# Performance work log

Hardware: AMD Instinct MI355X
Metric: run time of the kernel (lower is better)

Reference implementation:

```python
import jax, jax.numpy as jnp
import numpy as np

UNITS = 1024
INPUT_DIM = 2048
OUTPUT_DIM = 1000
EPS = 0.01
DT = 0.1
BATCH = 8192


def _kaiming_like(key, shape, fan_in):
    # matches torch kaiming_uniform_(a=sqrt(5)) bound = sqrt(6/((1+5)*fan_in)) = 1/sqrt(fan_in)
    bound = 1.0 / np.sqrt(fan_in)
    return jax.random.uniform(key, shape, jnp.float32, -bound, bound)


def setup_inputs() -> dict:
    key = jax.random.key(0)
    ks = jax.random.split(key, 12)
    x = jax.random.normal(ks[0], (BATCH, INPUT_DIM), jnp.float32)
    W_in = _kaiming_like(ks[1], (UNITS, INPUT_DIM), INPUT_DIM)
    b_in = _kaiming_like(ks[2], (UNITS,), INPUT_DIM)
    W1 = _kaiming_like(ks[3], (UNITS, UNITS), UNITS)
    b1 = _kaiming_like(ks[4], (UNITS,), UNITS)
    W2 = _kaiming_like(ks[5], (UNITS, UNITS), UNITS)
    b2 = _kaiming_like(ks[6], (UNITS,), UNITS)
    W3 = _kaiming_like(ks[7], (UNITS, UNITS), UNITS)
    b3 = _kaiming_like(ks[8], (UNITS,), UNITS)
    W_out = _kaiming_like(ks[9], (OUTPUT_DIM, UNITS), UNITS)
    b_out = _kaiming_like(ks[10], (OUTPUT_DIM,), UNITS)
    return {"x": x, "W_in": W_in, "b_in": b_in, "W1": W1, "b1": b1,
            "W2": W2, "b2": b2, "W3": W3, "b3": b3,
            "W_out": W_out, "b_out": b_out}


def transnet_layer(z, W, b):
    # z: (B, 2U). Implicit layer: A y = rhs, output = C y - rhs (== -y mathematically)
    U = W.shape[0]
    u_in, v_in = z[:, :U], z[:, U:]
    relu_u = jax.nn.relu(u_in)
    rhs_u = u_in + DT * b                      # (B, U)
    rhs_v = v_in + (DT / EPS) * relu_u         # (B, U)
    rhs = jnp.concatenate([rhs_u, rhs_v], axis=1)  # (B, 2U)
    eye = jnp.eye(U, dtype=z.dtype)
    A = jnp.block([[eye, DT * W],
                   [-DT * W.T, (1.0 + DT / EPS) * eye]])  # (2U, 2U), batch-independent
    # factor once, solve against all batch rhs columns at once
    y = jnp.linalg.solve(A, rhs.T).T           # (B, 2U)
    u, v = y[:, :U], y[:, U:]
    u_out = DT * (v @ W.T) - u_in - DT * b
    v_out = -DT * (u @ W) + (DT / EPS) * v - v_in - (DT / EPS) * relu_u
    return jnp.concatenate([u_out, v_out], axis=1)


def reference(x, W_in, b_in, W1, b1, W2, b2, W3, b3, W_out, b_out):
    z = x @ W_in.T + b_in                      # (B, U)
    z = jnp.concatenate([z, jax.nn.relu(z)], axis=1)  # (B, 2U)
    z = transnet_layer(z, W1, b1)
    z = transnet_layer(z, W2, b2)
    z = transnet_layer(z, W3, b3)
    z = z[:, :UNITS]
    logits = jax.nn.softmax(z @ W_out.T + b_out, axis=1)
    return logits
```

## Files before the change

kernel.cpp:

```cpp
#include <hip/hip_runtime.h>
#include <hip/hip_bf16.h>
#include <cstdint>


typedef __bf16 bf16;
typedef __bf16 bf16x4 __attribute__((ext_vector_type(4)));
typedef __bf16 bf16x8 __attribute__((ext_vector_type(8)));
typedef float  f32x4  __attribute__((ext_vector_type(4)));

#define C_DT    0.1f
#define C_DTEPS 10.0f
#define C_DINV  (1.0f/11.0f)
#define C_MSC   (0.01f/121.0f)

__device__ __forceinline__ void async_load16(const bf16* g, bf16* l) {
    __builtin_amdgcn_global_load_lds(
        (__attribute__((address_space(1))) void*)(g),
        (__attribute__((address_space(3))) void*)(l),
        16, 0, 0);
}

__device__ __forceinline__ void remap_block(int& bx, int& by) {
    if (gridDim.y == 64) {
        const int lin  = by * 8 + bx;
        const int xcd  = lin & 7;
        const int slot = lin >> 3;
        by = xcd * 8 + (slot & 7);
        bx = slot >> 3;
    }
}

template<int EPI>
__global__ __launch_bounds__(256, 3)
void gemm_bt(const bf16* __restrict__ A, const bf16* __restrict__ B,
             float* __restrict__ out_f,
             bf16* __restrict__ out_b1, bf16* __restrict__ out_b2,
             const float* __restrict__ e0, const float* __restrict__ e1,
             const float* __restrict__ e2,
             int M, int N, int K, int lda, int ldb,
             int ldf, int ld1, int ld2, float sgn,
             long zsA, long zsB, long zs1, long zs2)
{
    __shared__ __attribute__((aligned(16))) char smem[32768];
    bf16* sAe = (bf16*)smem;
    bf16* sBe = (bf16*)(smem + 16384);

    const int t    = threadIdx.x;
    const int wave = t >> 6;
    const int lane = t & 63;
    int bx = blockIdx.x, by = blockIdx.y;
    remap_block(bx, by);
    const long zb = blockIdx.z;
    A += zb * zsA;
    B += zb * zsB;
    if (out_b1) out_b1 += zb * zs1;
    if (out_b2) out_b2 += zb * zs2;

    const long row0 = (long)by * 128;
    const long col0 = (long)bx * 128;
    const int wr = wave >> 1, wc = wave & 1;

    f32x4 acc[4][4];
#pragma unroll
    for (int i = 0; i < 4; i++)
#pragma unroll
        for (int j = 0; j < 4; j++)
            acc[i][j] = f32x4{0.f, 0.f, 0.f, 0.f};

    const int  q  = t >> 2;
    const int  gp = ((t & 3) + 4 - ((q + (q >> 2)) & 3)) & 3;
    const bf16* gA = A + (row0 + q) * (long)lda + gp * 8;
    const bf16* gB = B + (col0 + q) * (long)ldb + gp * 8;

    const int l15  = lane & 15;
    const int fch  = ((lane >> 4) + l15 + (l15 >> 2)) & 3;
    const int aoff = (wr * 64 + l15) * 32 + fch * 8;
    const int boff = (wc * 64 + l15) * 32 + fch * 8;

    auto stage = [&](int buf, int k0) {
        bf16* dA = sAe + buf * 4096 + wave * 512;
        bf16* dB = sBe + buf * 4096 + wave * 512;
        async_load16(gA + k0,                     dA);
        async_load16(gA + 64 * (long)lda + k0,    dA + 2048);
        async_load16(gB + k0,                     dB);
        async_load16(gB + 64 * (long)ldb + k0,    dB + 2048);
    };

    const int nIter = K >> 5;
    stage(0, 0);
    __syncthreads();
    for (int k = 0; k < nIter; k++) {
        const int cur = k & 1;
        if (k + 1 < nIter) stage(cur ^ 1, (k + 1) << 5);

        bf16x8 af[4], bfv[4];
#pragma unroll
        for (int i = 0; i < 4; i++)
            af[i] = *(const bf16x8*)(sAe + cur * 4096 + aoff + i * 16 * 32);
#pragma unroll
        for (int j = 0; j < 4; j++)
            bfv[j] = *(const bf16x8*)(sBe + cur * 4096 + boff + j * 16 * 32);
#pragma unroll
        for (int i = 0; i < 4; i++)
#pragma unroll
            for (int j = 0; j < 4; j++)
                acc[i][j] = __builtin_amdgcn_mfma_f32_16x16x32_bf16(
                    af[i], bfv[j], acc[i][j], 0, 0, 0);

        __syncthreads();
    }

    float* epi = (float*)smem + wave * 1024;
    const int wbase = (lane >> 4) * 256 + (l15 >> 2) * 4 + (l15 & 3);

#pragma unroll
    for (int i = 0; i < 4; i++) {
#pragma unroll
        for (int j = 0; j < 4; j++)
#pragma unroll
            for (int r = 0; r < 4; r++)
                epi[wbase + r * 64 + 16 * j] = acc[i][j][r];

#pragma unroll
        for (int qq = 0; qq < 4; qq++) {
            const f32x4 a4 = ((const f32x4*)epi)[qq * 64 + lane];
            const long m = row0 + wr * 64 + i * 16 + qq * 4 + (lane >> 4);
            const long n = col0 + wc * 64 + 4 * l15;

            if (EPI == 0) {
                const f32x4 b1 = *(const f32x4*)(e1 + n);
                const f32x4 b2 = *(const f32x4*)(e2 + n);
                f32x4 tv; bf16x4 rv, hv;
#pragma unroll
                for (int e = 0; e < 4; e++) {
                    tv[e] = a4[e] + b1[e];
                    rv[e] = (bf16)(11.f * fmaxf(tv[e], 0.f));
                    hv[e] = (bf16)(tv[e] + C_DT * b2[e]);
                }
                *(f32x4*)(out_f + m * (long)ldf + n)    = tv;
                *(bf16x4*)(out_b1 + m * (long)ld1 + n)  = rv;
                *(bf16x4*)(out_b2 + m * (long)ld2 + n)  = hv;
            } else if (EPI == 1) {
                bf16x4 ov;
#pragma unroll
                for (int e = 0; e < 4; e++)
                    ov[e] = (bf16)(((m == n + e) ? C_DINV : 0.f) - C_MSC * a4[e]);
                *(bf16x4*)(out_b1 + m * (long)ld1 + n) = ov;
                *(bf16x4*)(out_b2 + m * (long)ld2 + n) = ov;
            } else if (EPI == 2) {
                bf16x4 ov, o2;
#pragma unroll
                for (int e = 0; e < 4; e++) {
                    ov[e] = (bf16)(sgn * a4[e]);
                    o2[e] = (bf16)(C_DT * sgn * a4[e]);
                }
                *(bf16x4*)(out_b1 + m * (long)ld1 + n) = ov;
                if (out_b2) *(bf16x4*)(out_b2 + m * (long)ld2 + n) = o2;
            } else {
                const f32x4 u0 = *(const f32x4*)(e0 + m * (long)ldf + n);
                const f32x4 b1 = *(const f32x4*)(e1 + n);
                bf16x4 hv, lv;
#pragma unroll
                for (int e = 0; e < 4; e++) {
                    float un = sgn * a4[e] - u0[e] - C_DT * b1[e];
                    bf16 h = (bf16)un;
                    hv[e] = h;
                    lv[e] = (bf16)(un - (float)h);
                }
                *(bf16x4*)(out_b1 + m * (long)ld1 + n) = hv;
                *(bf16x4*)(out_b2 + m * (long)ld2 + n) = lv;
            }
        }
    }
}

__global__ __launch_bounds__(256, 2)
void gemm_layer(const bf16* __restrict__ A, const bf16* __restrict__ B1,
                const bf16* __restrict__ B2, float* __restrict__ u,
                bf16* __restrict__ ACo,
                const float* __restrict__ bl, const float* __restrict__ bn)
{
    __shared__ __attribute__((aligned(16))) char smem[49152];
    bf16* sA  = (bf16*)smem;
    bf16* sB1 = (bf16*)(smem + 16384);
    bf16* sB2 = (bf16*)(smem + 32768);

    const int t    = threadIdx.x;
    const int wave = t >> 6;
    const int lane = t & 63;
    int bx = blockIdx.x, by = blockIdx.y;
    remap_block(bx, by);
    const long row0 = (long)by * 128;
    const long col0 = (long)bx * 128;
    const int wr = wave >> 1, wc = wave & 1;

    f32x4 accU[4][4], accV[4][4];
#pragma unroll
    for (int i = 0; i < 4; i++)
#pragma unroll
        for (int j = 0; j < 4; j++) {
            accU[i][j] = f32x4{0.f, 0.f, 0.f, 0.f};
            accV[i][j] = f32x4{0.f, 0.f, 0.f, 0.f};
        }

    const int  q  = t >> 2;
    const int  gp = ((t & 3) + 4 - ((q + (q >> 2)) & 3)) & 3;
    const bf16* gA  = A  + (row0 + q) * 2048 + gp * 8;
    const bf16* gB1 = B1 + (col0 + q) * 2048 + gp * 8;
    const bf16* gB2 = B2 + (col0 + q) * 2048 + gp * 8;

    const int l15  = lane & 15;
    const int fch  = ((lane >> 4) + l15 + (l15 >> 2)) & 3;
    const int aoff = (wr * 64 + l15) * 32 + fch * 8;
    const int boff = (wc * 64 + l15) * 32 + fch * 8;

    auto stage = [&](int buf, int k0) {
        bf16* dA  = sA  + buf * 4096 + wave * 512;
        bf16* dB1 = sB1 + buf * 4096 + wave * 512;
        bf16* dB2 = sB2 + buf * 4096 + wave * 512;
        async_load16(gA  + k0,             dA);
        async_load16(gA  + 64 * 2048 + k0, dA + 2048);
        async_load16(gB1 + k0,             dB1);
        async_load16(gB1 + 64 * 2048 + k0, dB1 + 2048);
        async_load16(gB2 + k0,             dB2);
        async_load16(gB2 + 64 * 2048 + k0, dB2 + 2048);
    };

    stage(0, 0);
    __syncthreads();
    for (int k = 0; k < 64; k++) {
        const int cur = k & 1;
        if (k + 1 < 64) stage(cur ^ 1, (k + 1) << 5);

        bf16x8 af[4], b1v[4], b2v[4];
#pragma unroll
        for (int i = 0; i < 4; i++)
            af[i] = *(const bf16x8*)(sA + cur * 4096 + aoff + i * 16 * 32);
#pragma unroll
        for (int j = 0; j < 4; j++) {
            b1v[j] = *(const bf16x8*)(sB1 + cur * 4096 + boff + j * 16 * 32);
            b2v[j] = *(const bf16x8*)(sB2 + cur * 4096 + boff + j * 16 * 32);
        }
#pragma unroll
        for (int i = 0; i < 4; i++)
#pragma unroll
            for (int j = 0; j < 4; j++) {
                accV[i][j] = __builtin_amdgcn_mfma_f32_16x16x32_bf16(
                    af[i], b1v[j], accV[i][j], 0, 0, 0);
                accU[i][j] = __builtin_amdgcn_mfma_f32_16x16x32_bf16(
                    af[i], b2v[j], accU[i][j], 0, 0, 0);
            }
        __syncthreads();
    }

    float* epi = (float*)smem + wave * 1024;
    const int wbase = (lane >> 4) * 256 + (l15 >> 2) * 4 + (l15 & 3);

#pragma unroll
    for (int i = 0; i < 4; i++) {
#pragma unroll
        for (int j = 0; j < 4; j++)
#pragma unroll
            for (int r = 0; r < 4; r++)
                epi[wbase + r * 64 + 16 * j] = accV[i][j][r];
        f32x4 v4[4];
#pragma unroll
        for (int qq = 0; qq < 4; qq++)
            v4[qq] = ((const f32x4*)epi)[qq * 64 + lane];
#pragma unroll
        for (int j = 0; j < 4; j++)
#pragma unroll
            for (int r = 0; r < 4; r++)
                epi[wbase + r * 64 + 16 * j] = accU[i][j][r];

#pragma unroll
        for (int qq = 0; qq < 4; qq++) {
            const f32x4 a4 = ((const f32x4*)epi)[qq * 64 + lane];
            const long m  = row0 + wr * 64 + i * 16 + qq * 4 + (lane >> 4);
            const long n  = col0 + wc * 64 + 4 * l15;
            const long iu = m * 1024 + n;
            const f32x4 u0 = *(const f32x4*)(u + iu);
            const f32x4 c1 = *(const f32x4*)(bl + n);
            const f32x4 c2 = *(const f32x4*)(bn + n);
            f32x4 un; bf16x4 rv, hv;
#pragma unroll
            for (int e = 0; e < 4; e++) {
                un[e] = a4[e] - u0[e] - C_DT * c1[e];
                rv[e] = (bf16)(C_DTEPS * fmaxf(un[e], 0.f) - v4[qq][e]);
                hv[e] = (bf16)(un[e] + C_DT * c2[e]);
            }
            *(f32x4*)(u + iu) = un;
            *(bf16x4*)(ACo + m * 2048 + n)        = rv;
            *(bf16x4*)(ACo + m * 2048 + 1024 + n) = hv;
        }
    }
}

__global__ __launch_bounds__(256, 3)
void gemm_step67(const bf16* __restrict__ Minv, const bf16* __restrict__ Wbf,
                 bf16* __restrict__ Bc1, bf16* __restrict__ Pm,
                 bf16* __restrict__ Cc)
{
    __shared__ __attribute__((aligned(16))) char smem[32768];
    bf16* sAe = (bf16*)smem;
    bf16* sBe = (bf16*)(smem + 16384);

    const int t    = threadIdx.x;
    const int wave = t >> 6;
    const int lane = t & 63;
    const int bx = blockIdx.x, by = blockIdx.y;
    const long zb = blockIdx.z;
    const long M1v = 1024L * 1024;

    const bf16 *A, *B;
    bf16 *o1, *o2;
    int ld1;
    const bool alt = (zb >= 3);
    if (!alt) {
        A = Minv + zb * M1v; B = Wbf + zb * M1v;
        o1 = Bc1 + zb * 2 * M1v; o2 = nullptr; ld1 = 2048;
    } else {
        const long zr = zb - 3;
        A = Wbf + zr * M1v; B = Minv + zr * M1v;
        o1 = Pm + zr * M1v; o2 = Cc + zr * 2 * M1v; ld1 = 1024;
    }

    const long row0 = (long)by * 128;
    const long col0 = (long)bx * 128;
    const int wr = wave >> 1, wc = wave & 1;

    f32x4 acc[4][4];
#pragma unroll
    for (int i = 0; i < 4; i++)
#pragma unroll
        for (int j = 0; j < 4; j++)
            acc[i][j] = f32x4{0.f, 0.f, 0.f, 0.f};

    const int  q  = t >> 2;
    const int  gp = ((t & 3) + 4 - ((q + (q >> 2)) & 3)) & 3;
    const bf16* gA = A + (row0 + q) * 1024 + gp * 8;
    const bf16* gB = B + (col0 + q) * 1024 + gp * 8;

    const int l15  = lane & 15;
    const int fch  = ((lane >> 4) + l15 + (l15 >> 2)) & 3;
    const int aoff = (wr * 64 + l15) * 32 + fch * 8;
    const int boff = (wc * 64 + l15) * 32 + fch * 8;

    auto stage = [&](int buf, int k0) {
        bf16* dA = sAe + buf * 4096 + wave * 512;
        bf16* dB = sBe + buf * 4096 + wave * 512;
        async_load16(gA + k0,              dA);
        async_load16(gA + 64 * 1024 + k0,  dA + 2048);
        async_load16(gB + k0,              dB);
        async_load16(gB + 64 * 1024 + k0,  dB + 2048);
    };

    stage(0, 0);
    __syncthreads();
    for (int k = 0; k < 32; k++) {
        const int cur = k & 1;
        if (k + 1 < 32) stage(cur ^ 1, (k + 1) << 5);

        bf16x8 af[4], bfv[4];
#pragma unroll
        for (int i = 0; i < 4; i++)
            af[i] = *(const bf16x8*)(sAe + cur * 4096 + aoff + i * 16 * 32);
#pragma unroll
        for (int j = 0; j < 4; j++)
            bfv[j] = *(const bf16x8*)(sBe + cur * 4096 + boff + j * 16 * 32);
#pragma unroll
        for (int i = 0; i < 4; i++)
#pragma unroll
            for (int j = 0; j < 4; j++)
                acc[i][j] = __builtin_amdgcn_mfma_f32_16x16x32_bf16(
                    af[i], bfv[j], acc[i][j], 0, 0, 0);
        __syncthreads();
    }

    float* epi = (float*)smem + wave * 1024;
    const int wbase = (lane >> 4) * 256 + (l15 >> 2) * 4 + (l15 & 3);

#pragma unroll
    for (int i = 0; i < 4; i++) {
#pragma unroll
        for (int j = 0; j < 4; j++)
#pragma unroll
            for (int r = 0; r < 4; r++)
                epi[wbase + r * 64 + 16 * j] = acc[i][j][r];

#pragma unroll
        for (int qq = 0; qq < 4; qq++) {
            const f32x4 a4 = ((const f32x4*)epi)[qq * 64 + lane];
            const long m = row0 + wr * 64 + i * 16 + qq * 4 + (lane >> 4);
            const long n = col0 + wc * 64 + 4 * l15;
            if (!alt) {
                bf16x4 ov;
#pragma unroll
                for (int e = 0; e < 4; e++) ov[e] = (bf16)(C_DT * a4[e]);
                *(bf16x4*)(o1 + m * (long)ld1 + n) = ov;
            } else {
                bf16x4 ov, o2v;
#pragma unroll
                for (int e = 0; e < 4; e++) {
                    ov[e]  = (bf16)a4[e];
                    o2v[e] = (bf16)(C_DT * a4[e]);
                }
                *(bf16x4*)(o1 + m * (long)ld1 + n) = ov;
                *(bf16x4*)(o2 + m * 2048 + n)      = o2v;
            }
        }
    }
}

__global__ __launch_bounds__(256, 2)
void gemm_split(const bf16* __restrict__ Ah, const bf16* __restrict__ Al,
                const bf16* __restrict__ Bh, const bf16* __restrict__ Bl,
                float* __restrict__ out, const float* __restrict__ bias,
                int M, int N, int K, int blim)
{
    __shared__ __attribute__((aligned(16))) char smem[65536];
    bf16* sAh = (bf16*)smem;
    bf16* sAl = (bf16*)(smem + 16384);
    bf16* sBh = (bf16*)(smem + 32768);
    bf16* sBl = (bf16*)(smem + 49152);

    const int t    = threadIdx.x;
    const int wave = t >> 6;
    const int lane = t & 63;
    int bx = blockIdx.x, by = blockIdx.y;
    remap_block(bx, by);
    const long row0 = (long)by * 128;
    const long col0 = (long)bx * 128;
    const int wr = wave >> 1, wc = wave & 1;

    f32x4 acc[4][4];
#pragma unroll
    for (int i = 0; i < 4; i++)
#pragma unroll
        for (int j = 0; j < 4; j++)
            acc[i][j] = f32x4{0.f, 0.f, 0.f, 0.f};

    const int  q  = t >> 2;
    const int  gp = ((t & 3) + 4 - ((q + (q >> 2)) & 3)) & 3;
    const long gao = (row0 + q) * (long)K + gp * 8;
    const long gbo = (col0 + q) * (long)K + gp * 8;

    const int l15  = lane & 15;
    const int fch  = ((lane >> 4) + l15 + (l15 >> 2)) & 3;
    const int aoff = (wr * 64 + l15) * 32 + fch * 8;
    const int boff = (wc * 64 + l15) * 32 + fch * 8;

    auto stage = [&](int buf, int k0) {
        const int d = buf * 4096 + wave * 512;
        async_load16(Ah + gao + k0,                 sAh + d);
        async_load16(Ah + gao + 64 * (long)K + k0,  sAh + d + 2048);
        async_load16(Al + gao + k0,                 sAl + d);
        async_load16(Al + gao + 64 * (long)K + k0,  sAl + d + 2048);
        async_load16(Bh + gbo + k0,                 sBh + d);
        async_load16(Bh + gbo + 64 * (long)K + k0,  sBh + d + 2048);
        async_load16(Bl + gbo + k0,                 sBl + d);
        async_load16(Bl + gbo + 64 * (long)K + k0,  sBl + d + 2048);
    };

    const int nIter = K >> 5;
    stage(0, 0);
    __syncthreads();
    for (int k = 0; k < nIter; k++) {
        const int cur = k & 1;
        if (k + 1 < nIter) stage(cur ^ 1, (k + 1) << 5);

        bf16x8 ah[4], al[4], bh[4], bl[4];
#pragma unroll
        for (int i = 0; i < 4; i++) {
            ah[i] = *(const bf16x8*)(sAh + cur * 4096 + aoff + i * 16 * 32);
            al[i] = *(const bf16x8*)(sAl + cur * 4096 + aoff + i * 16 * 32);
        }
#pragma unroll
        for (int j = 0; j < 4; j++) {
            bh[j] = *(const bf16x8*)(sBh + cur * 4096 + boff + j * 16 * 32);
            bl[j] = *(const bf16x8*)(sBl + cur * 4096 + boff + j * 16 * 32);
        }
#pragma unroll
        for (int i = 0; i < 4; i++)
#pragma unroll
            for (int j = 0; j < 4; j++) {
                acc[i][j] = __builtin_amdgcn_mfma_f32_16x16x32_bf16(
                    ah[i], bh[j], acc[i][j], 0, 0, 0);
                acc[i][j] = __builtin_amdgcn_mfma_f32_16x16x32_bf16(
                    ah[i], bl[j], acc[i][j], 0, 0, 0);
                acc[i][j] = __builtin_amdgcn_mfma_f32_16x16x32_bf16(
                    al[i], bh[j], acc[i][j], 0, 0, 0);
            }
        __syncthreads();
    }

    float* epi = (float*)smem + wave * 1024;
    const int wbase = (lane >> 4) * 256 + (l15 >> 2) * 4 + (l15 & 3);

#pragma unroll
    for (int i = 0; i < 4; i++) {
#pragma unroll
        for (int j = 0; j < 4; j++)
#pragma unroll
            for (int r = 0; r < 4; r++)
                epi[wbase + r * 64 + 16 * j] = acc[i][j][r];

#pragma unroll
        for (int qq = 0; qq < 4; qq++) {
            f32x4 a4 = ((const f32x4*)epi)[qq * 64 + lane];
            const long m = row0 + wr * 64 + i * 16 + qq * 4 + (lane >> 4);
            const long n = col0 + wc * 64 + 4 * l15;
            f32x4 bv = f32x4{0.f, 0.f, 0.f, 0.f};
            if (n < blim) bv = *(const f32x4*)(bias + n);
#pragma unroll
            for (int e = 0; e < 4; e++) a4[e] += bv[e];
            *(f32x4*)(out + m * (long)N + n) = a4;
        }
    }
}

__global__ __launch_bounds__(256)
void prep_all(const float* __restrict__ x, bf16* __restrict__ xb,
              const float* __restrict__ win, bf16* __restrict__ winb,
              const float* __restrict__ wout, bf16* __restrict__ wouth,
              bf16* __restrict__ woutl,
              const float* __restrict__ w0, const float* __restrict__ w1,
              const float* __restrict__ w2,
              bf16* __restrict__ Wb, bf16* __restrict__ Wtb)
{
    __shared__ float tile[32][33];
    const long bid = blockIdx.x;
    const int  t   = threadIdx.x;

    if (bid < 16384) {
        const long i4 = bid * 256 + t;
        const f32x4 v = ((const f32x4*)x)[i4];
        bf16x4 o;
#pragma unroll
        for (int e = 0; e < 4; e++) o[e] = (bf16)v[e];
        ((bf16x4*)xb)[i4] = o;
    } else if (bid < 18432) {
        const long i4 = (bid - 16384) * 256 + t;
        const f32x4 v = ((const f32x4*)win)[i4];
        bf16x4 o;
#pragma unroll
        for (int e = 0; e < 4; e++) o[e] = (bf16)v[e];
        ((bf16x4*)winb)[i4] = o;
    } else if (bid < 19456) {
        const long i4   = (bid - 18432) * 256 + t;
        const long base = i4 * 4;
        const int  nrow = (int)(base >> 10);
        bf16x4 h, l;
        if (nrow < 1000) {
            const f32x4 v = ((const f32x4*)wout)[i4];
#pragma unroll
            for (int e = 0; e < 4; e++) {
                bf16 hh = (bf16)v[e];
                h[e] = hh;
                l[e] = (bf16)(v[e] - (float)hh);
            }
        } else {
#pragma unroll
            for (int e = 0; e < 4; e++) { h[e] = (bf16)0.f; l[e] = (bf16)0.f; }
        }
        ((bf16x4*)wouth)[i4] = h;
        ((bf16x4*)woutl)[i4] = l;
    } else {
        const long b2 = bid - 19456;
        const int  z  = (int)(b2 >> 10);
        const int  idx = (int)(b2 & 1023);
        const float* W = (z == 0) ? w0 : (z == 1) ? w1 : w2;
        const long zo = (long)z << 20;
        const int bxt = (idx & 31) * 32, byt = (idx >> 5) * 32;
        const int tx = t & 31, ty = t >> 5;
#pragma unroll
        for (int i = 0; i < 32; i += 8) {
            float v = W[(long)(byt + ty + i) * 1024 + bxt + tx];
            tile[ty + i][tx] = v;
            Wb[zo + (long)(byt + ty + i) * 1024 + bxt + tx] = (bf16)v;
        }
        __syncthreads();
#pragma unroll
        for (int i = 0; i < 32; i += 8)
            Wtb[zo + (long)(bxt + ty + i) * 1024 + byt + tx] = (bf16)tile[tx][ty + i];
    }
}

__global__ __launch_bounds__(256)
void softmax_rows(const float* __restrict__ logits, float* __restrict__ out)
{
    const int row = blockIdx.x;
    const float* lp = logits + (long)row * 1024;
    const int t = threadIdx.x;
    float v[4];
    float mx = -1e30f;
#pragma unroll
    for (int i = 0; i < 4; i++) {
        const int c = t + i * 256;
        v[i] = (c < 1000) ? lp[c] : -1e30f;
        mx = fmaxf(mx, v[i]);
    }
#pragma unroll
    for (int off = 32; off; off >>= 1)
        mx = fmaxf(mx, __shfl_xor(mx, off));
    __shared__ float sm[4], ss[4];
    const int wave = t >> 6;
    if ((t & 63) == 0) sm[wave] = mx;
    __syncthreads();
    mx = fmaxf(fmaxf(sm[0], sm[1]), fmaxf(sm[2], sm[3]));
    float sum = 0.f;
#pragma unroll
    for (int i = 0; i < 4; i++) {
        v[i] = __expf(v[i] - mx);
        sum += v[i];
    }
#pragma unroll
    for (int off = 32; off; off >>= 1)
        sum += __shfl_xor(sum, off);
    if ((t & 63) == 0) ss[wave] = sum;
    __syncthreads();
    const float inv = 1.f / (ss[0] + ss[1] + ss[2] + ss[3]);
#pragma unroll
    for (int i = 0; i < 4; i++) {
        const int c = t + i * 256;
        if (c < 1000) out[(long)row * 1000 + c] = v[i] * inv;
    }
}

extern "C" void kernel_launch(void* const* d_in, const int* in_sizes, int n_in,
                              void* d_out, int out_size, void* d_ws, size_t ws_size,
                              hipStream_t stream)
{
    const float* x     = (const float*)d_in[0];
    const float* W_in  = (const float*)d_in[1];
    const float* b_in  = (const float*)d_in[2];
    const float* Ws[3] = {(const float*)d_in[3], (const float*)d_in[5], (const float*)d_in[7]};
    const float* bs[3] = {(const float*)d_in[4], (const float*)d_in[6], (const float*)d_in[8]};
    const float* W_out = (const float*)d_in[9];
    const float* b_out = (const float*)d_in[10];
    float* out = (float*)d_out;

    char* ws = (char*)d_ws;
    const size_t MB = 1u << 20;
    const long M1 = 1024L * 1024;
    bf16*  xb    = (bf16*)(ws);
    bf16*  Minv  = (bf16*)(ws +  6 * MB);
    bf16*  Pmat  = (bf16*)(ws + 12 * MB);
    bf16*  Bcat  = (bf16*)(ws + 18 * MB);
    bf16*  zh    = (bf16*)(ws);
    bf16*  zl    = (bf16*)(ws + 16 * MB);
    bf16*  Winb  = (bf16*)(ws + 32 * MB);
    bf16*  Wouth = (bf16*)(ws + 36 * MB);
    bf16*  Woutl = (bf16*)(ws + 38 * MB);
    bf16*  Wbf   = (bf16*)(ws + 40 * MB);
    bf16*  Ccat  = (bf16*)(ws + 46 * MB);
    float* u     = (float*)(ws + 58 * MB);
    float* logits= (float*)(ws + 58 * MB);
    bf16*  AC_a  = (bf16*)(ws + 90 * MB);
    bf16*  AC_b  = (bf16*)(ws + 122 * MB);
    bf16*  Wtbf  = (bf16*)(ws + 122 * MB);

    const dim3 blk(256);
    const dim3 gBig(8, 64);
    const dim3 gSm3(8, 8, 3);
    const dim3 gSm6(8, 8, 6);

    prep_all<<<22528, blk, 0, stream>>>(x, xb, W_in, Winb, W_out, Wouth, Woutl,
                                        Ws[0], Ws[1], Ws[2], Wbf, Wtbf);

    gemm_bt<0><<<gBig, blk, 0, stream>>>(xb, Winb, u, AC_a, AC_a + 1024,
                                         nullptr, b_in, bs[0],
                                         8192, 1024, 2048, 2048, 2048,
                                         1024, 2048, 2048, 1.f, 0, 0, 0, 0);

    gemm_bt<1><<<gSm3, blk, 0, stream>>>(Wtbf, Wtbf, nullptr, Minv, Bcat,
                                         nullptr, nullptr, nullptr,
                                         1024, 1024, 1024, 1024, 1024,
                                         0, 1024, 2048, 1.f, M1, M1, M1, 2 * M1);
    gemm_step67<<<gSm6, blk, 0, stream>>>(Minv, Wbf, Bcat + 1024, Pmat, Ccat);
    gemm_bt<2><<<gSm3, blk, 0, stream>>>(Pmat, Wbf, nullptr, Ccat + 1024, nullptr,
                                         nullptr, nullptr, nullptr,
                                         1024, 1024, 1024, 1024, 1024,
                                         0, 2048, 0, 0.01f, M1, M1, 2 * M1, 0);

    gemm_layer<<<gBig, blk, 0, stream>>>(AC_a, Bcat, Ccat, u, AC_b, bs[0], bs[1]);
    gemm_layer<<<gBig, blk, 0, stream>>>(AC_b, Bcat + 2 * M1, Ccat + 2 * M1,
                                         u, AC_a, bs[1], bs[2]);
    gemm_bt<5><<<gBig, blk, 0, stream>>>(AC_a, Ccat + 4 * M1, nullptr, zh, zl,
                                         u, bs[2], nullptr,
                                         8192, 1024, 2048, 2048, 2048,
                                         1024, 1024, 1024, 1.f, 0, 0, 0, 0);

    gemm_split<<<gBig, blk, 0, stream>>>(zh, zl, Wouth, Woutl, logits, b_out,
                                         8192, 1024, 1024, 1000);
    softmax_rows<<<8192, blk, 0, stream>>>(logits, out);
}
```

Baseline: 515.3 us.

## Compute layer U from materialized V via W instead of separate wide GEMM

Each implicit layer is split into two GEMMs. The first computes V with K=2048 and writes it to a bf16 buffer. The second GEMM has K=1024 and multiplies V by W to get the U term, scaled by DT in the epilogue. This replaces the fused dual-accumulator GEMM, which computed both halves over K=2048 each, and it cuts precomputation of the Pmat/Ccat matrices to only the final layer's slice. The cost is an extra bf16 round trip of V through global memory, one more kernel launch per layer, and V being rounded to bf16 before it feeds U, which can reduce accuracy.

```diff
diff --git a/kernel.cpp b/kernel.cpp
--- a/kernel.cpp
+++ b/kernel.cpp
@@ -174,16 +174,14 @@
     }
 }
 
-__global__ __launch_bounds__(256, 2)
-void gemm_layer(const bf16* __restrict__ A, const bf16* __restrict__ B1,
-                const bf16* __restrict__ B2, float* __restrict__ u,
-                bf16* __restrict__ ACo,
-                const float* __restrict__ bl, const float* __restrict__ bn)
+__global__ __launch_bounds__(256, 3)
+void gemm_ulayer(const bf16* __restrict__ V, const bf16* __restrict__ W,
+                 float* __restrict__ u, bf16* __restrict__ ACo,
+                 const float* __restrict__ bl, const float* __restrict__ bn)
 {
-    __shared__ __attribute__((aligned(16))) char smem[49152];
-    bf16* sA  = (bf16*)smem;
-    bf16* sB1 = (bf16*)(smem + 16384);
-    bf16* sB2 = (bf16*)(smem + 32768);
+    __shared__ __attribute__((aligned(16))) char smem[32768];
+    bf16* sAe = (bf16*)smem;
+    bf16* sBe = (bf16*)(smem + 16384);
 
     const int t    = threadIdx.x;
     const int wave = t >> 6;
@@ -194,20 +192,17 @@
     const long col0 = (long)bx * 128;
     const int wr = wave >> 1, wc = wave & 1;
 
-    f32x4 accU[4][4], accV[4][4];
+    f32x4 acc[4][4];
 #pragma unroll
     for (int i = 0; i < 4; i++)
 #pragma unroll
-        for (int j = 0; j < 4; j++) {
-            accU[i][j] = f32x4{0.f, 0.f, 0.f, 0.f};
-            accV[i][j] = f32x4{0.f, 0.f, 0.f, 0.f};
-        }
+        for (int j = 0; j < 4; j++)
+            acc[i][j] = f32x4{0.f, 0.f, 0.f, 0.f};
 
     const int  q  = t >> 2;
     const int  gp = ((t & 3) + 4 - ((q + (q >> 2)) & 3)) & 3;
-    const bf16* gA  = A  + (row0 + q) * 2048 + gp * 8;
-    const bf16* gB1 = B1 + (col0 + q) * 2048 + gp * 8;
-    const bf16* gB2 = B2 + (col0 + q) * 2048 + gp * 8;
+    const bf16* gA = V + (row0 + q) * 1024 + gp * 8;
+    const bf16* gB = W + (col0 + q) * 1024 + gp * 8;
 
     const int l15  = lane & 15;
     const int fch  = ((lane >> 4) + l15 + (l15 >> 2)) & 3;
@@ -215,41 +210,33 @@
     const int boff = (wc * 64 + l15) * 32 + fch * 8;
 
     auto stage = [&](int buf, int k0) {
-        bf16* dA  = sA  + buf * 4096 + wave * 512;
-        bf16* dB1 = sB1 + buf * 4096 + wave * 512;
-        bf16* dB2 = sB2 + buf * 4096 + wave * 512;
-        async_load16(gA  + k0,             dA);
-        async_load16(gA  + 64 * 2048 + k0, dA + 2048);
-        async_load16(gB1 + k0,             dB1);
-        async_load16(gB1 + 64 * 2048 + k0, dB1 + 2048);
-        async_load16(gB2 + k0,             dB2);
-        async_load16(gB2 + 64 * 2048 + k0, dB2 + 2048);
+        bf16* dA = sAe + buf * 4096 + wave * 512;
+        bf16* dB = sBe + buf * 4096 + wave * 512;
+        async_load16(gA + k0,              dA);
+        async_load16(gA + 64 * 1024 + k0,  dA + 2048);
+        async_load16(gB + k0,              dB);
+        async_load16(gB + 64 * 1024 + k0,  dB + 2048);
     };
 
     stage(0, 0);
     __syncthreads();
-    for (int k = 0; k < 64; k++) {
+    for (int k = 0; k < 32; k++) {
         const int cur = k & 1;
-        if (k + 1 < 64) stage(cur ^ 1, (k + 1) << 5);
-
-        bf16x8 af[4], b1v[4], b2v[4];
+        if (k + 1 < 32) stage(cur ^ 1, (k + 1) << 5);
+
+        bf16x8 af[4], bfv[4];
 #pragma unroll
         for (int i = 0; i < 4; i++)
-            af[i] = *(const bf16x8*)(sA + cur * 4096 + aoff + i * 16 * 32);
-#pragma unroll
-        for (int j = 0; j < 4; j++) {
-            b1v[j] = *(const bf16x8*)(sB1 + cur * 4096 + boff + j * 16 * 32);
-            b2v[j] = *(const bf16x8*)(sB2 + cur * 4096 + boff + j * 16 * 32);
-        }
+            af[i] = *(const bf16x8*)(sAe + cur * 4096 + aoff + i * 16 * 32);
+#pragma unroll
+        for (int j = 0; j < 4; j++)
+            bfv[j] = *(const bf16x8*)(sBe + cur * 4096 + boff + j * 16 * 32);
 #pragma unroll
         for (int i = 0; i < 4; i++)
 #pragma unroll
-            for (int j = 0; j < 4; j++) {
-                accV[i][j] = __builtin_amdgcn_mfma_f32_16x16x32_bf16(
-                    af[i], b1v[j], accV[i][j], 0, 0, 0);
-                accU[i][j] = __builtin_amdgcn_mfma_f32_16x16x32_bf16(
-                    af[i], b2v[j], accU[i][j], 0, 0, 0);
-            }
+            for (int j = 0; j < 4; j++)
+                acc[i][j] = __builtin_amdgcn_mfma_f32_16x16x32_bf16(
+                    af[i], bfv[j], acc[i][j], 0, 0, 0);
         __syncthreads();
     }
 
@@ -262,16 +249,7 @@
         for (int j = 0; j < 4; j++)
 #pragma unroll
             for (int r = 0; r < 4; r++)
-                epi[wbase + r * 64 + 16 * j] = accV[i][j][r];
-        f32x4 v4[4];
-#pragma unroll
-        for (int qq = 0; qq < 4; qq++)
-            v4[qq] = ((const f32x4*)epi)[qq * 64 + lane];
-#pragma unroll
-        for (int j = 0; j < 4; j++)
-#pragma unroll
-            for (int r = 0; r < 4; r++)
-                epi[wbase + r * 64 + 16 * j] = accU[i][j][r];
+                epi[wbase + r * 64 + 16 * j] = acc[i][j][r];
 
 #pragma unroll
         for (int qq = 0; qq < 4; qq++) {
@@ -279,14 +257,15 @@
             const long m  = row0 + wr * 64 + i * 16 + qq * 4 + (lane >> 4);
             const long n  = col0 + wc * 64 + 4 * l15;
             const long iu = m * 1024 + n;
-            const f32x4 u0 = *(const f32x4*)(u + iu);
-            const f32x4 c1 = *(const f32x4*)(bl + n);
-            const f32x4 c2 = *(const f32x4*)(bn + n);
+            const f32x4  u0 = *(const f32x4*)(u + iu);
+            const f32x4  c1 = *(const f32x4*)(bl + n);
+            const f32x4  c2 = *(const f32x4*)(bn + n);
+            const bf16x4 vv = *(const bf16x4*)(V + iu);
             f32x4 un; bf16x4 rv, hv;
 #pragma unroll
             for (int e = 0; e < 4; e++) {
-                un[e] = a4[e] - u0[e] - C_DT * c1[e];
-                rv[e] = (bf16)(C_DTEPS * fmaxf(un[e], 0.f) - v4[qq][e]);
+                un[e] = C_DT * a4[e] - u0[e] - C_DT * c1[e];
+                rv[e] = (bf16)(C_DTEPS * fmaxf(un[e], 0.f) - (float)vv[e]);
                 hv[e] = (bf16)(un[e] + C_DT * c2[e]);
             }
             *(f32x4*)(u + iu) = un;
@@ -315,14 +294,13 @@
     const bf16 *A, *B;
     bf16 *o1, *o2;
     int ld1;
-    const bool alt = (zb >= 3);
+    const bool alt = (zb >= 2);
     if (!alt) {
         A = Minv + zb * M1v; B = Wbf + zb * M1v;
         o1 = Bc1 + zb * 2 * M1v; o2 = nullptr; ld1 = 2048;
     } else {
-        const long zr = zb - 3;
-        A = Wbf + zr * M1v; B = Minv + zr * M1v;
-        o1 = Pm + zr * M1v; o2 = Cc + zr * 2 * M1v; ld1 = 1024;
+        A = Wbf + 2 * M1v; B = Minv + 2 * M1v;
+        o1 = Pm; o2 = Cc; ld1 = 1024;
     }
 
     const long row0 = (long)by * 128;
@@ -644,6 +622,7 @@
     const size_t MB = 1u << 20;
     const long M1 = 1024L * 1024;
     bf16*  xb    = (bf16*)(ws);
+    bf16*  Vbuf  = (bf16*)(ws);
     bf16*  Minv  = (bf16*)(ws +  6 * MB);
     bf16*  Pmat  = (bf16*)(ws + 12 * MB);
     bf16*  Bcat  = (bf16*)(ws + 18 * MB);
@@ -663,7 +642,7 @@
     const dim3 blk(256);
     const dim3 gBig(8, 64);
     const dim3 gSm3(8, 8, 3);
-    const dim3 gSm6(8, 8, 6);
+    const dim3 gSm1(8, 8, 1);
 
     prep_all<<<22528, blk, 0, stream>>>(x, xb, W_in, Winb, W_out, Wouth, Woutl,
                                         Ws[0], Ws[1], Ws[2], Wbf, Wtbf);
@@ -677,16 +656,25 @@
                                          nullptr, nullptr, nullptr,
                                          1024, 1024, 1024, 1024, 1024,
                                          0, 1024, 2048, 1.f, M1, M1, M1, 2 * M1);
-    gemm_step67<<<gSm6, blk, 0, stream>>>(Minv, Wbf, Bcat + 1024, Pmat, Ccat);
-    gemm_bt<2><<<gSm3, blk, 0, stream>>>(Pmat, Wbf, nullptr, Ccat + 1024, nullptr,
+    gemm_step67<<<gSm3, blk, 0, stream>>>(Minv, Wbf, Bcat + 1024, Pmat, Ccat);
+    gemm_bt<2><<<gSm1, blk, 0, stream>>>(Pmat, Wbf + 2 * M1, nullptr,
+                                         Ccat + 1024, nullptr,
                                          nullptr, nullptr, nullptr,
                                          1024, 1024, 1024, 1024, 1024,
-                                         0, 2048, 0, 0.01f, M1, M1, 2 * M1, 0);
-
-    gemm_layer<<<gBig, blk, 0, stream>>>(AC_a, Bcat, Ccat, u, AC_b, bs[0], bs[1]);
-    gemm_layer<<<gBig, blk, 0, stream>>>(AC_b, Bcat + 2 * M1, Ccat + 2 * M1,
-                                         u, AC_a, bs[1], bs[2]);
-    gemm_bt<5><<<gBig, blk, 0, stream>>>(AC_a, Ccat + 4 * M1, nullptr, zh, zl,
+                                         0, 2048, 0, 0.01f, 0, 0, 0, 0);
+
+    gemm_bt<2><<<gBig, blk, 0, stream>>>(AC_a, Bcat, nullptr, Vbuf, nullptr,
+                                         nullptr, nullptr, nullptr,
+                                         8192, 1024, 2048, 2048, 2048,
+                                         0, 1024, 0, 1.f, 0, 0, 0, 0);
+    gemm_ulayer<<<gBig, blk, 0, stream>>>(Vbuf, Wbf, u, AC_b, bs[0], bs[1]);
+    gemm_bt<2><<<gBig, blk, 0, stream>>>(AC_b, Bcat + 2 * M1, nullptr, Vbuf, nullptr,
+                                         nullptr, nullptr, nullptr,
+                                         8192, 1024, 2048, 2048, 2048,
+                                         0, 1024, 0, 1.f, 0, 0, 0, 0);
+    gemm_ulayer<<<gBig, blk, 0, stream>>>(Vbuf, Wbf + M1, u, AC_a, bs[1], bs[2]);
+
+    gemm_bt<5><<<gBig, blk, 0, stream>>>(AC_a, Ccat, nullptr, zh, zl,
                                          u, bs[2], nullptr,
                                          8192, 1024, 2048, 2048, 2048,
                                          1024, 1024, 1024, 1.f, 0, 0, 0, 0);
```

New measurement: 531.0 us. +3.1%, slower.

## Merge first-layer and matrix-inverse GEMMs; fuse prep GEMMs via atomic dependency counter

Applied to the files above, without the earlier changes.

Runs the input projection GEMM and the three per-layer Minv Gram GEMMs in one launch, with block roles chosen by blockIdx.y, so the small 1024x1024 GEMMs fill idle CUs alongside the big one. It also collapses the step67 and EPI2 GEMMs into a single persistent-style launch. Consumer blocks spin on a global atomic counter until all 384 producer blocks have finished. Producer blocks also copy Minv into the Bcat high half, replacing the duplicate write in the old epilogue. This removes several launches and tail effects, but the spin-wait assumes producer blocks are scheduled before consumers and can deadlock if they are not; it also adds a memset.

```diff
diff --git a/kernel.cpp b/kernel.cpp
--- a/kernel.cpp
+++ b/kernel.cpp
@@ -127,36 +127,7 @@
             const long m = row0 + wr * 64 + i * 16 + qq * 4 + (lane >> 4);
             const long n = col0 + wc * 64 + 4 * l15;
 
-            if (EPI == 0) {
-                const f32x4 b1 = *(const f32x4*)(e1 + n);
-                const f32x4 b2 = *(const f32x4*)(e2 + n);
-                f32x4 tv; bf16x4 rv, hv;
-#pragma unroll
-                for (int e = 0; e < 4; e++) {
-                    tv[e] = a4[e] + b1[e];
-                    rv[e] = (bf16)(11.f * fmaxf(tv[e], 0.f));
-                    hv[e] = (bf16)(tv[e] + C_DT * b2[e]);
-                }
-                *(f32x4*)(out_f + m * (long)ldf + n)    = tv;
-                *(bf16x4*)(out_b1 + m * (long)ld1 + n)  = rv;
-                *(bf16x4*)(out_b2 + m * (long)ld2 + n)  = hv;
-            } else if (EPI == 1) {
-                bf16x4 ov;
-#pragma unroll
-                for (int e = 0; e < 4; e++)
-                    ov[e] = (bf16)(((m == n + e) ? C_DINV : 0.f) - C_MSC * a4[e]);
-                *(bf16x4*)(out_b1 + m * (long)ld1 + n) = ov;
-                *(bf16x4*)(out_b2 + m * (long)ld2 + n) = ov;
-            } else if (EPI == 2) {
-                bf16x4 ov, o2;
-#pragma unroll
-                for (int e = 0; e < 4; e++) {
-                    ov[e] = (bf16)(sgn * a4[e]);
-                    o2[e] = (bf16)(C_DT * sgn * a4[e]);
-                }
-                *(bf16x4*)(out_b1 + m * (long)ld1 + n) = ov;
-                if (out_b2) *(bf16x4*)(out_b2 + m * (long)ld2 + n) = o2;
-            } else {
+            if (EPI == 5) {
                 const f32x4 u0 = *(const f32x4*)(e0 + m * (long)ldf + n);
                 const f32x4 b1 = *(const f32x4*)(e1 + n);
                 bf16x4 hv, lv;
@@ -171,6 +142,284 @@
                 *(bf16x4*)(out_b2 + m * (long)ld2 + n) = lv;
             }
         }
+    }
+}
+
+__global__ __launch_bounds__(256, 3)
+void gemm_z0m(const bf16* __restrict__ xb, const bf16* __restrict__ winb,
+              const bf16* __restrict__ wtbf,
+              float* __restrict__ u, bf16* __restrict__ ACa,
+              bf16* __restrict__ Minv,
+              const float* __restrict__ e1, const float* __restrict__ e2)
+{
+    __shared__ __attribute__((aligned(16))) char smem[32768];
+    bf16* sAe = (bf16*)smem;
+    bf16* sBe = (bf16*)(smem + 16384);
+
+    const int t    = threadIdx.x;
+    const int wave = t >> 6;
+    const int lane = t & 63;
+    const long M1v = 1024L * 1024;
+
+    const bool mainp = (blockIdx.y < 64);
+    int bx, by, nIter, zm = 0;
+    long lda;
+    const bf16 *Abase, *Bbase;
+    if (mainp) {
+        const int lin  = blockIdx.y * 8 + blockIdx.x;
+        const int xcd  = lin & 7;
+        const int slot = lin >> 3;
+        by = xcd * 8 + (slot & 7);
+        bx = slot >> 3;
+        lda = 2048; nIter = 64;
+        Abase = xb; Bbase = winb;
+    } else {
+        zm = (blockIdx.y - 64) >> 3;
+        by = (blockIdx.y - 64) & 7;
+        bx = blockIdx.x;
+        lda = 1024; nIter = 32;
+        Abase = wtbf + zm * M1v; Bbase = Abase;
+    }
+    const long row0 = (long)by * 128;
+    const long col0 = (long)bx * 128;
+    const int wr = wave >> 1, wc = wave & 1;
+
+    f32x4 acc[4][4];
+#pragma unroll
+    for (int i = 0; i < 4; i++)
+#pragma unroll
+        for (int j = 0; j < 4; j++)
+            acc[i][j] = f32x4{0.f, 0.f, 0.f, 0.f};
+
+    const int  q  = t >> 2;
+    const int  gp = ((t & 3) + 4 - ((q + (q >> 2)) & 3)) & 3;
+    const bf16* gA = Abase + (row0 + q) * lda + gp * 8;
+    const bf16* gB = Bbase + (col0 + q) * lda + gp * 8;
+
+    const int l15  = lane & 15;
+    const int fch  = ((lane >> 4) + l15 + (l15 >> 2)) & 3;
+    const int aoff = (wr * 64 + l15) * 32 + fch * 8;
+    const int boff = (wc * 64 + l15) * 32 + fch * 8;
+
+    auto stage = [&](int buf, int k0) {
+        bf16* dA = sAe + buf * 4096 + wave * 512;
+        bf16* dB = sBe + buf * 4096 + wave * 512;
+        async_load16(gA + k0,              dA);
+        async_load16(gA + 64 * lda + k0,   dA + 2048);
+        async_load16(gB + k0,              dB);
+        async_load16(gB + 64 * lda + k0,   dB + 2048);
+    };
+
+    stage(0, 0);
+    __syncthreads();
+    for (int k = 0; k < nIter; k++) {
+        const int cur = k & 1;
+        if (k + 1 < nIter) stage(cur ^ 1, (k + 1) << 5);
+
+        bf16x8 af[4], bfv[4];
+#pragma unroll
+        for (int i = 0; i < 4; i++)
+            af[i] = *(const bf16x8*)(sAe + cur * 4096 + aoff + i * 16 * 32);
+#pragma unroll
+        for (int j = 0; j < 4; j++)
+            bfv[j] = *(const bf16x8*)(sBe + cur * 4096 + boff + j * 16 * 32);
+#pragma unroll
+        for (int i = 0; i < 4; i++)
+#pragma unroll
+            for (int j = 0; j < 4; j++)
+                acc[i][j] = __builtin_amdgcn_mfma_f32_16x16x32_bf16(
+                    af[i], bfv[j], acc[i][j], 0, 0, 0);
+        __syncthreads();
+    }
+
+    float* epi = (float*)smem + wave * 1024;
+    const int wbase = (lane >> 4) * 256 + (l15 >> 2) * 4 + (l15 & 3);
+
+#pragma unroll
+    for (int i = 0; i < 4; i++) {
+#pragma unroll
+        for (int j = 0; j < 4; j++)
+#pragma unroll
+            for (int r = 0; r < 4; r++)
+                epi[wbase + r * 64 + 16 * j] = acc[i][j][r];
+
+#pragma unroll
+        for (int qq = 0; qq < 4; qq++) {
+            const f32x4 a4 = ((const f32x4*)epi)[qq * 64 + lane];
+            const long m = row0 + wr * 64 + i * 16 + qq * 4 + (lane >> 4);
+            const long n = col0 + wc * 64 + 4 * l15;
+
+            if (mainp) {
+                const f32x4 b1 = *(const f32x4*)(e1 + n);
+                const f32x4 b2 = *(const f32x4*)(e2 + n);
+                f32x4 tv; bf16x4 rv, hv;
+#pragma unroll
+                for (int e = 0; e < 4; e++) {
+                    tv[e] = a4[e] + b1[e];
+                    rv[e] = (bf16)(11.f * fmaxf(tv[e], 0.f));
+                    hv[e] = (bf16)(tv[e] + C_DT * b2[e]);
+                }
+                *(f32x4*)(u + m * 1024 + n)           = tv;
+                *(bf16x4*)(ACa + m * 2048 + n)        = rv;
+                *(bf16x4*)(ACa + m * 2048 + 1024 + n) = hv;
+            } else {
+                bf16x4 ov;
+#pragma unroll
+                for (int e = 0; e < 4; e++)
+                    ov[e] = (bf16)(((m == n + e) ? C_DINV : 0.f) - C_MSC * a4[e]);
+                *(bf16x4*)(Minv + zm * M1v + m * 1024 + n) = ov;
+            }
+        }
+    }
+}
+
+__global__ __launch_bounds__(256, 3)
+void pp2(const bf16* __restrict__ Minv, const bf16* __restrict__ Wbf,
+         bf16* __restrict__ Bcat, bf16* __restrict__ Pmat,
+         bf16* __restrict__ Ccat, unsigned int* __restrict__ ctr)
+{
+    __shared__ __attribute__((aligned(16))) char smem[32768];
+    bf16* sAe = (bf16*)smem;
+    bf16* sBe = (bf16*)(smem + 16384);
+
+    const int bid  = blockIdx.x;
+    const int t    = threadIdx.x;
+    const int wave = t >> 6;
+    const int lane = t & 63;
+    const long M1v = 1024L * 1024;
+    const bool prod = (bid < 384);
+
+    const bf16 *A, *B;
+    bf16 *o1, *o2 = nullptr;
+    bf16 *bhi = nullptr;
+    int ld1 = 2048, bx, by;
+    float s1, s2 = C_DT;
+
+    if (prod) {
+        const int z6  = bid >> 6;
+        const int idx = bid & 63;
+        bx = idx & 7; by = idx >> 3;
+        if (z6 < 3) {
+            A = Minv + z6 * M1v; B = Wbf + z6 * M1v;
+            o1 = Bcat + z6 * 2 * M1v + 1024; s1 = C_DT;
+            bhi = Bcat + z6 * 2 * M1v;
+        } else {
+            const int zr = z6 - 3;
+            A = Wbf + zr * M1v; B = Minv + zr * M1v;
+            o1 = Pmat + zr * M1v; ld1 = 1024; s1 = 1.f;
+            o2 = Ccat + zr * 2 * M1v;
+        }
+    } else {
+        if (t == 0) {
+            while (__hip_atomic_load(ctr, __ATOMIC_ACQUIRE,
+                                     __HIP_MEMORY_SCOPE_AGENT) < 384u)
+                __builtin_amdgcn_s_sleep(8);
+        }
+        __syncthreads();
+        const int idx2 = bid - 384;
+        const int zc   = idx2 >> 6;
+        const int idx  = idx2 & 63;
+        bx = idx & 7; by = idx >> 3;
+        A = Pmat + zc * M1v; B = Wbf + zc * M1v;
+        o1 = Ccat + zc * 2 * M1v + 1024; s1 = 0.01f;
+    }
+
+    const long row0 = (long)by * 128;
+    const long col0 = (long)bx * 128;
+    const int wr = wave >> 1, wc = wave & 1;
+
+    if (bhi) {
+        const int rr = t >> 1, cc = (t & 1) * 64;
+#pragma unroll
+        for (int s = 0; s < 8; s++) {
+            const long src = (row0 + rr) * 1024 + col0 + cc + s * 8;
+            *(bf16x8*)(bhi + (row0 + rr) * 2048 + col0 + cc + s * 8) =
+                *(const bf16x8*)(A + src);
+        }
+    }
+
+    f32x4 acc[4][4];
+#pragma unroll
+    for (int i = 0; i < 4; i++)
+#pragma unroll
+        for (int j = 0; j < 4; j++)
+            acc[i][j] = f32x4{0.f, 0.f, 0.f, 0.f};
+
+    const int  q  = t >> 2;
+    const int  gp = ((t & 3) + 4 - ((q + (q >> 2)) & 3)) & 3;
+    const bf16* gA = A + (row0 + q) * 1024 + gp * 8;
+    const bf16* gB = B + (col0 + q) * 1024 + gp * 8;
+
+    const int l15  = lane & 15;
+    const int fch  = ((lane >> 4) + l15 + (l15 >> 2)) & 3;
+    const int aoff = (wr * 64 + l15) * 32 + fch * 8;
+    const int boff = (wc * 64 + l15) * 32 + fch * 8;
+
+    auto stage = [&](int buf, int k0) {
+        bf16* dA = sAe + buf * 4096 + wave * 512;
+        bf16* dB = sBe + buf * 4096 + wave * 512;
+        async_load16(gA + k0,              dA);
+        async_load16(gA + 64 * 1024 + k0,  dA + 2048);
+        async_load16(gB + k0,              dB);
+        async_load16(gB + 64 * 1024 + k0,  dB + 2048);
+    };
+
+    stage(0, 0);
+    __syncthreads();
+    for (int k = 0; k < 32; k++) {
+        const int cur = k & 1;
+        if (k + 1 < 32) stage(cur ^ 1, (k + 1) << 5);
+
+        bf16x8 af[4], bfv[4];
+#pragma unroll
+        for (int i = 0; i < 4; i++)
+            af[i] = *(const bf16x8*)(sAe + cur * 4096 + aoff + i * 16 * 32);
+#pragma unroll
+        for (int j = 0; j < 4; j++)
+            bfv[j] = *(const bf16x8*)(sBe + cur * 4096 + boff + j * 16 * 32);
+#pragma unroll
+        for (int i = 0; i < 4; i++)
+#pragma unroll
+            for (int j = 0; j < 4; j++)
+                acc[i][j] = __builtin_amdgcn_mfma_f32_16x16x32_bf16(
+                    af[i], bfv[j], acc[i][j], 0, 0, 0);
+        __syncthreads();
+    }
+
+    float* epi = (float*)smem + wave * 1024;
+    const int wbase = (lane >> 4) * 256 + (l15 >> 2) * 4 + (l15 & 3);
+
+#pragma unroll
+    for (int i = 0; i < 4; i++) {
+#pragma unroll
+        for (int j = 0; j < 4; j++)
+#pragma unroll
+            for (int r = 0; r < 4; r++)
+                epi[wbase + r * 64 + 16 * j] = acc[i][j][r];
+
+#pragma unroll
+        for (int qq = 0; qq < 4; qq++) {
+            const f32x4 a4 = ((const f32x4*)epi)[qq * 64 + lane];
+            const long m = row0 + wr * 64 + i * 16 + qq * 4 + (lane >> 4);
+            const long n = col0 + wc * 64 + 4 * l15;
+            bf16x4 ov;
+#pragma unroll
+            for (int e = 0; e < 4; e++) ov[e] = (bf16)(s1 * a4[e]);
+            *(bf16x4*)(o1 + m * (long)ld1 + n) = ov;
+            if (o2) {
+                bf16x4 o2v;
+#pragma unroll
+                for (int e = 0; e < 4; e++) o2v[e] = (bf16)(s2 * a4[e]);
+                *(bf16x4*)(o2 + m * 2048 + n) = o2v;
+            }
+        }
+    }
+
+    if (prod) {
+        __syncthreads();
+        if (t == 0)
+            __hip_atomic_fetch_add(ctr, 1u, __ATOMIC_RELEASE,
+                                   __HIP_MEMORY_SCOPE_AGENT);
     }
 }
 
@@ -292,122 +541,6 @@
             *(f32x4*)(u + iu) = un;
             *(bf16x4*)(ACo + m * 2048 + n)        = rv;
             *(bf16x4*)(ACo + m * 2048 + 1024 + n) = hv;
-        }
-    }
-}
-
-__global__ __launch_bounds__(256, 3)
-void gemm_step67(const bf16* __restrict__ Minv, const bf16* __restrict__ Wbf,
-                 bf16* __restrict__ Bc1, bf16* __restrict__ Pm,
-                 bf16* __restrict__ Cc)
-{
-    __shared__ __attribute__((aligned(16))) char smem[32768];
-    bf16* sAe = (bf16*)smem;
-    bf16* sBe = (bf16*)(smem + 16384);
-
-    const int t    = threadIdx.x;
-    const int wave = t >> 6;
-    const int lane = t & 63;
-    const int bx = blockIdx.x, by = blockIdx.y;
-    const long zb = blockIdx.z;
-    const long M1v = 1024L * 1024;
-
-    const bf16 *A, *B;
-    bf16 *o1, *o2;
-    int ld1;
-    const bool alt = (zb >= 3);
-    if (!alt) {
-        A = Minv + zb * M1v; B = Wbf + zb * M1v;
-        o1 = Bc1 + zb * 2 * M1v; o2 = nullptr; ld1 = 2048;
-    } else {
-        const long zr = zb - 3;
-        A = Wbf + zr * M1v; B = Minv + zr * M1v;
-        o1 = Pm + zr * M1v; o2 = Cc + zr * 2 * M1v; ld1 = 1024;
-    }
-
-    const long row0 = (long)by * 128;
-    const long col0 = (long)bx * 128;
-    const int wr = wave >> 1, wc = wave & 1;
-
-    f32x4 acc[4][4];
-#pragma unroll
-    for (int i = 0; i < 4; i++)
-#pragma unroll
-        for (int j = 0; j < 4; j++)
-            acc[i][j] = f32x4{0.f, 0.f, 0.f, 0.f};
-
-    const int  q  = t >> 2;
-    const int  gp = ((t & 3) + 4 - ((q + (q >> 2)) & 3)) & 3;
-    const bf16* gA = A + (row0 + q) * 1024 + gp * 8;
-    const bf16* gB = B + (col0 + q) * 1024 + gp * 8;
-
-    const int l15  = lane & 15;
-    const int fch  = ((lane >> 4) + l15 + (l15 >> 2)) & 3;
-    const int aoff = (wr * 64 + l15) * 32 + fch * 8;
-    const int boff = (wc * 64 + l15) * 32 + fch * 8;
-
-    auto stage = [&](int buf, int k0) {
-        bf16* dA = sAe + buf * 4096 + wave * 512;
-        bf16* dB = sBe + buf * 4096 + wave * 512;
-        async_load16(gA + k0,              dA);
-        async_load16(gA + 64 * 1024 + k0,  dA + 2048);
-        async_load16(gB + k0,              dB);
-        async_load16(gB + 64 * 1024 + k0,  dB + 2048);
-    };
-
-    stage(0, 0);
-    __syncthreads();
-    for (int k = 0; k < 32; k++) {
-        const int cur = k & 1;
-        if (k + 1 < 32) stage(cur ^ 1, (k + 1) << 5);
-
-        bf16x8 af[4], bfv[4];
-#pragma unroll
-        for (int i = 0; i < 4; i++)
-            af[i] = *(const bf16x8*)(sAe + cur * 4096 + aoff + i * 16 * 32);
-#pragma unroll
-        for (int j = 0; j < 4; j++)
-            bfv[j] = *(const bf16x8*)(sBe + cur * 4096 + boff + j * 16 * 32);
-#pragma unroll
-        for (int i = 0; i < 4; i++)
-#pragma unroll
-            for (int j = 0; j < 4; j++)
-                acc[i][j] = __builtin_amdgcn_mfma_f32_16x16x32_bf16(
-                    af[i], bfv[j], acc[i][j], 0, 0, 0);
-        __syncthreads();
-    }
-
-    float* epi = (float*)smem + wave * 1024;
-    const int wbase = (lane >> 4) * 256 + (l15 >> 2) * 4 + (l15 & 3);
-
-#pragma unroll
-    for (int i = 0; i < 4; i++) {
-#pragma unroll
-        for (int j = 0; j < 4; j++)
-#pragma unroll
-            for (int r = 0; r < 4; r++)
-                epi[wbase + r * 64 + 16 * j] = acc[i][j][r];
-
-#pragma unroll
-        for (int qq = 0; qq < 4; qq++) {
-            const f32x4 a4 = ((const f32x4*)epi)[qq * 64 + lane];
-            const long m = row0 + wr * 64 + i * 16 + qq * 4 + (lane >> 4);
-            const long n = col0 + wc * 64 + 4 * l15;
-            if (!alt) {
-                bf16x4 ov;
-#pragma unroll
-                for (int e = 0; e < 4; e++) ov[e] = (bf16)(C_DT * a4[e]);
-                *(bf16x4*)(o1 + m * (long)ld1 + n) = ov;
-            } else {
-                bf16x4 ov, o2v;
-#pragma unroll
-                for (int e = 0; e < 4; e++) {
-                    ov[e]  = (bf16)a4[e];
-                    o2v[e] = (bf16)(C_DT * a4[e]);
-                }
-                *(bf16x4*)(o1 + m * (long)ld1 + n) = ov;
-                *(bf16x4*)(o2 + m * 2048 + n)      = o2v;
-            }
         }
     }
 }
@@ -644,11 +777,9 @@
     const size_t MB = 1u << 20;
     const long M1 = 1024L * 1024;
     bf16*  xb    = (bf16*)(ws);
-    bf16*  Minv  = (bf16*)(ws +  6 * MB);
-    bf16*  Pmat  = (bf16*)(ws + 12 * MB);
-    bf16*  Bcat  = (bf16*)(ws + 18 * MB);
     bf16*  zh    = (bf16*)(ws);
     bf16*  zl    = (bf16*)(ws + 16 * MB);
+    bf16*  Bcat  = (bf16*)(ws + 18 * MB);
     bf16*  Winb  = (bf16*)(ws + 32 * MB);
     bf16*  Wouth = (bf16*)(ws + 36 * MB);
     bf16*  Woutl = (bf16*)(ws + 38 * MB);
@@ -659,29 +790,23 @@
     bf16*  AC_a  = (bf16*)(ws + 90 * MB);
     bf16*  AC_b  = (bf16*)(ws + 122 * MB);
     bf16*  Wtbf  = (bf16*)(ws + 122 * MB);
+    bf16*  Minv  = (bf16*)(ws + 128 * MB);
+    bf16*  Pmat  = (bf16*)(ws + 134 * MB);
+    unsigned int* ctr = (unsigned int*)(ws + 140 * MB);
 
     const dim3 blk(256);
     const dim3 gBig(8, 64);
-    const dim3 gSm3(8, 8, 3);
-    const dim3 gSm6(8, 8, 6);
+    const dim3 gZ0(8, 88);
+
+    hipMemsetAsync(ctr, 0, 64, stream);
 
     prep_all<<<22528, blk, 0, stream>>>(x, xb, W_in, Winb, W_out, Wouth, Woutl,
                                         Ws[0], Ws[1], Ws[2], Wbf, Wtbf);
 
-    gemm_bt<0><<<gBig, blk, 0, stream>>>(xb, Winb, u, AC_a, AC_a + 1024,
-                                         nullptr, b_in, bs[0],
-                                         8192, 1024, 2048, 2048, 2048,
-                                         1024, 2048, 2048, 1.f, 0, 0, 0, 0);
-
-    gemm_bt<1><<<gSm3, blk, 0, stream>>>(Wtbf, Wtbf, nullptr, Minv, Bcat,
-                                         nullptr, nullptr, nullptr,
-                                         1024, 1024, 1024, 1024, 1024,
-                                         0, 1024, 2048, 1.f, M1, M1, M1, 2 * M1);
-    gemm_step67<<<gSm6, blk, 0, stream>>>(Minv, Wbf, Bcat + 1024, Pmat, Ccat);
-    gemm_bt<2><<<gSm3, blk, 0, stream>>>(Pmat, Wbf, nullptr, Ccat + 1024, nullptr,
-                                         nullptr, nullptr, nullptr,
-                                         1024, 1024, 1024, 1024, 1024,
-                                         0, 2048, 0, 0.01f, M1, M1, 2 * M1, 0);
+    gemm_z0m<<<gZ0, blk, 0, stream>>>(xb, Winb, Wtbf, u, AC_a, Minv,
+                                      b_in, bs[0]);
+
+    pp2<<<576, blk, 0, stream>>>(Minv, Wbf, Bcat, Pmat, Ccat, ctr);
 
     gemm_layer<<<gBig, blk, 0, stream>>>(AC_a, Bcat, Ccat, u, AC_b, bs[0], bs[1]);
     gemm_layer<<<gBig, blk, 0, stream>>>(AC_b, Bcat + 2 * M1, Ccat + 2 * M1,
```

Result: slower. 608.1 us (+18.0%).
